# Optimization experiments

Measured on AMD Instinct MI355X. Metric: run time of the kernel, lower is better.

## Reference

```python
import jax, jax.numpy as jnp
import numpy as np

BATCH = 32
LATENT = 128
NODE_DIM = 8
MAX_NODES = 512
H_NODE = 128   # node_generator hidden
H_EDGE = 64    # edge_generator hidden


def setup_inputs() -> dict:
    key = jax.random.key(0)
    ks = jax.random.split(key, 9)
    s = 0.02
    return {
        "z":   jax.random.normal(ks[0], (BATCH, LATENT), dtype=jnp.float32),
        "W1":  jax.random.normal(ks[1], (LATENT, H_NODE), dtype=jnp.float32) * s,
        "b1":  jnp.zeros((H_NODE,), dtype=jnp.float32),
        "W2":  jax.random.normal(ks[2], (H_NODE, MAX_NODES * NODE_DIM), dtype=jnp.float32) * s,
        "b2":  jnp.zeros((MAX_NODES * NODE_DIM,), dtype=jnp.float32),
        "E1":  jax.random.normal(ks[3], (2 * NODE_DIM, H_EDGE), dtype=jnp.float32) * s,
        "eb1": jnp.zeros((H_EDGE,), dtype=jnp.float32),
        "E2":  jax.random.normal(ks[4], (H_EDGE, 1), dtype=jnp.float32) * s,
        "eb2": jnp.zeros((1,), dtype=jnp.float32),
    }


def reference(z, W1, b1, W2, b2, E1, eb1, E2, eb2):
    B = z.shape[0]
    # node generator: Linear -> ReLU -> Linear, view to [B, N, node_dim]
    h = jax.nn.relu(z @ W1 + b1)
    nodes = (h @ W2 + b2).reshape(B, MAX_NODES, NODE_DIM)

    # all unordered pairs i < j (static indices)
    iu, ju = np.triu_indices(MAX_NODES, k=1)  # [P]
    pair = jnp.concatenate([nodes[:, iu, :], nodes[:, ju, :]], axis=-1)  # [B, P, 2d]

    # edge generator: Linear -> ReLU -> Linear -> Sigmoid
    he = jax.nn.relu(jnp.einsum("bpd,dh->bph", pair, E1) + eb1)
    p = jax.nn.sigmoid(jnp.einsum("bph,ho->bpo", he, E2) + eb2)[..., 0]  # [B, P]

    adj = jnp.zeros((B, MAX_NODES, MAX_NODES), dtype=p.dtype)
    adj = adj.at[:, iu, ju].set(p).at[:, ju, iu].set(p)
    return nodes, adj
```

## Files before the change

kernel.cpp:

```cpp
#include <hip/hip_runtime.h>

#define BATCH 32
#define LATENT 128
#define NODE_DIM 8
#define MAX_NODES 512
#define H_NODE 128
#define H_EDGE 64

typedef _Float16 h2 __attribute__((ext_vector_type(2)));

static __device__ __forceinline__ h2 u32_to_h2(unsigned int x) {
    union { unsigned int u; h2 h; } c; c.u = x; return c.h;
}
static __device__ __forceinline__ unsigned int h2_to_u32(h2 x) {
    union { unsigned int u; h2 h; } c; c.h = x; return c.u;
}

#if __has_builtin(__builtin_amdgcn_fdot2)
#define FDOT2(a, b, c) __builtin_amdgcn_fdot2((a), (b), (c), false)
#else
#define FDOT2(a, b, c) ((c) + (float)(a).x * (float)(b).x + (float)(a).y * (float)(b).y)
#endif

#define UPKH_DWORDS (BATCH * 32 * MAX_NODES)

__global__ __launch_bounds__(256) void gen_nodes_uv(
    const float* __restrict__ z,  const float* __restrict__ W1,
    const float* __restrict__ b1, const float* __restrict__ W2,
    const float* __restrict__ b2, const float* __restrict__ E1,
    const float* __restrict__ eb1,
    float* __restrict__ nodes_out, unsigned int* __restrict__ UPKH,
    unsigned int* __restrict__ VH)
{
    const int b      = blockIdx.x;
    const int mslice = blockIdx.y;
    const int tid    = threadIdx.x;
    const int i0     = mslice * 32;

    __shared__ float sz[LATENT];
    __shared__ float sh[H_NODE];
    __shared__ float sE1[2 * NODE_DIM][H_EDGE];
    __shared__ float sEb1[H_EDGE];
    __shared__ float sN[32][NODE_DIM];

    if (tid < LATENT) sz[tid] = z[b * LATENT + tid];
    for (int idx = tid; idx < 2 * NODE_DIM * H_EDGE; idx += 256)
        (&sE1[0][0])[idx] = E1[idx];
    if (tid < H_EDGE) sEb1[tid] = eb1[tid];
    __syncthreads();

    if (tid < H_NODE) {
        float acc = b1[tid];
#pragma unroll 8
        for (int k = 0; k < LATENT; ++k)
            acc += sz[k] * W1[k * H_NODE + tid];
        sh[tid] = fmaxf(acc, 0.0f);
    }
    __syncthreads();

    const int m = mslice * 256 + tid;
    float acc = b2[m];
#pragma unroll 8
    for (int k = 0; k < H_NODE; ++k)
        acc += sh[k] * W2[(size_t)k * (MAX_NODES * NODE_DIM) + m];
    nodes_out[(size_t)b * (MAX_NODES * NODE_DIM) + m] = acc;
    sN[tid >> 3][tid & 7] = acc;
    __syncthreads();

    {
        const int il = tid & 31;
        const int cg = tid >> 5;
#pragma unroll
        for (int rep = 0; rep < 4; ++rep) {
            const int c2 = rep * 8 + cg;
            const int c  = 2 * c2;
            float ua = sEb1[c], ub = sEb1[c + 1];
#pragma unroll
            for (int d = 0; d < NODE_DIM; ++d) {
                const float nd = sN[il][d];
                ua += nd * sE1[d][c];
                ub += nd * sE1[d][c + 1];
            }
            h2 uu = { (_Float16)ua, (_Float16)ub };
            UPKH[((size_t)b * 32 + c2) * MAX_NODES + i0 + il] = h2_to_u32(uu);
        }
    }
    {
        const int jl = tid >> 3;
        const int cq = tid & 7;
#pragma unroll
        for (int rep = 0; rep < 4; ++rep) {
            const int c2 = rep * 8 + cq;
            const int c  = 2 * c2;
            float va = 0.f, vb = 0.f;
#pragma unroll
            for (int d = 0; d < NODE_DIM; ++d) {
                const float nd = sN[jl][d];
                va += nd * sE1[NODE_DIM + d][c];
                vb += nd * sE1[NODE_DIM + d][c + 1];
            }
            h2 vv = { (_Float16)va, (_Float16)vb };
            VH[((size_t)(b * MAX_NODES + i0 + jl) << 5) + c2] = h2_to_u32(vv);
        }
    }
}

__global__ __launch_bounds__(256, 6) void edge_gen(
    const unsigned int* __restrict__ UPKH, const unsigned int* __restrict__ VH,
    const float* __restrict__ E2,  const float* __restrict__ eb2,
    float* __restrict__ adj)
{
    const int b = blockIdx.y;
    int t = blockIdx.x, bi = 0;
    while (t >= 16 - 2 * bi) { t -= 16 - 2 * bi; ++bi; }
    const int jt = 2 * bi + t;
    const bool partial = (jt >> 1) == bi;

    const int tid  = threadIdx.x;
    const int lane = tid & 63;
    const int wv   = tid >> 6;
    const int i0 = bi * 64, j0 = jt * 32;
    const int i  = i0 + lane;

    __shared__ float P[32][65];

    unsigned int uA[32];
#pragma unroll
    for (int c2 = 0; c2 < 32; ++c2)
        uA[c2] = UPKH[((size_t)b * 32 + c2) * MAX_NODES + i];

    unsigned int wb[32];
#pragma unroll
    for (int c2 = 0; c2 < 32; ++c2) {
        h2 w = { (_Float16)E2[2 * c2], (_Float16)E2[2 * c2 + 1] };
        wb[c2] = __builtin_amdgcn_readfirstlane(h2_to_u32(w));
    }

    const float bias = eb2[0];
    float* adjb = adj + (size_t)b * MAX_NODES * MAX_NODES;
    const h2 zh = { (_Float16)0.f, (_Float16)0.f };

#pragma unroll 2
    for (int jj = 0; jj < 8; ++jj) {
        const int jl = wv * 8 + jj;
        const int j  = j0 + jl;
        const int jfl = __builtin_amdgcn_readfirstlane(j);
        const uint4* vrow = (const uint4*)(VH + ((size_t)(b * MAX_NODES + jfl) << 5));

        float a0 = 0.f, a1 = 0.f;
#pragma unroll
        for (int q = 0; q < 8; ++q) {
            const uint4 vv = vrow[q];
#pragma unroll
            for (int k = 0; k < 4; ++k) {
                const int c2 = 4 * q + k;
                unsigned int vu = (k == 0) ? vv.x : (k == 1) ? vv.y
                                : (k == 2) ? vv.z : vv.w;
                const h2 v = u32_to_h2(vu);
                const h2 w = u32_to_h2(wb[c2]);
                h2 s = u32_to_h2(uA[c2]) + v;
                s = __builtin_elementwise_max(s, zh);
                if (k & 1) a1 = FDOT2(s, w, a1);
                else       a0 = FDOT2(s, w, a0);
            }
        }
        const float x = a0 + a1 + bias;
        const float p = __builtin_amdgcn_rcpf(1.0f + __expf(-x));

        if (!partial) {
            adjb[(size_t)j * MAX_NODES + i] = p;
            P[jl][lane] = p;
        } else {
            if (i < j)       { adjb[(size_t)j * MAX_NODES + i] = p;
                               adjb[(size_t)i * MAX_NODES + j] = p; }
            else if (i == j)   adjb[(size_t)j * MAX_NODES + i] = 0.0f;
        }
    }

    if (!partial) {
        __syncthreads();
        const int r = tid & 63;
        const int q = tid >> 6;
        const size_t rowbase = (size_t)(i0 + r) * MAX_NODES + j0 + q * 8;
        float4 o0, o1;
        o0.x = P[q * 8 + 0][r]; o0.y = P[q * 8 + 1][r];
        o0.z = P[q * 8 + 2][r]; o0.w = P[q * 8 + 3][r];
        o1.x = P[q * 8 + 4][r]; o1.y = P[q * 8 + 5][r];
        o1.z = P[q * 8 + 6][r]; o1.w = P[q * 8 + 7][r];
        *(float4*)&adjb[rowbase]     = o0;
        *(float4*)&adjb[rowbase + 4] = o1;
    }
}

extern "C" void kernel_launch(void* const* d_in, const int* in_sizes, int n_in,
                              void* d_out, int out_size, void* d_ws, size_t ws_size,
                              hipStream_t stream)
{
    const float* z   = (const float*)d_in[0];
    const float* W1  = (const float*)d_in[1];
    const float* b1  = (const float*)d_in[2];
    const float* W2  = (const float*)d_in[3];
    const float* b2  = (const float*)d_in[4];
    const float* E1  = (const float*)d_in[5];
    const float* eb1 = (const float*)d_in[6];
    const float* E2  = (const float*)d_in[7];
    const float* eb2 = (const float*)d_in[8];

    float* nodes_out = (float*)d_out;
    float* adj       = (float*)d_out + BATCH * MAX_NODES * NODE_DIM;

    unsigned int* UPKH = (unsigned int*)d_ws;
    unsigned int* VHp  = UPKH + UPKH_DWORDS;

    dim3 g1(BATCH, 16);
    gen_nodes_uv<<<g1, 256, 0, stream>>>(z, W1, b1, W2, b2, E1, eb1,
                                         nodes_out, UPKH, VHp);

    dim3 g2(72, BATCH);
    edge_gen<<<g2, 256, 0, stream>>>(UPKH, VHp, E2, eb2, adj);
}
```

Baseline: 47.91 us.

## Process three tiles per edge block with U reuse and precomputed E2 halves

The edge kernel grid shrinks from 72 to 24 blocks per batch. Each block now walks three tiles taken from a constant tile table and reloads the U registers only when the row tile changes, so per-block setup is amortized. The fp16 conversion of E2 moves into the node kernel and is written to workspace. The trade-off is fewer blocks (768 total) with less latency hiding, an extra barrier per tile, and dropping the occupancy hint from launch_bounds.

```diff
diff --git a/kernel.cpp b/kernel.cpp
--- a/kernel.cpp
+++ b/kernel.cpp
@@ -23,14 +23,26 @@
 #endif
 
 #define UPKH_DWORDS (BATCH * 32 * MAX_NODES)
+#define VH_DWORDS   (BATCH * MAX_NODES * 32)
+
+__device__ const unsigned char TILE_CODE[72] = {
+    0x00,0x01,0x02,0x03,0x04,0x05,0x06,0x07,0x08,0x09,0x0A,0x0B,0x0C,0x0D,0x0E,0x0F,
+    0x12,0x13,0x14,0x15,0x16,0x17,0x18,0x19,0x1A,0x1B,0x1C,0x1D,0x1E,0x1F,
+    0x24,0x25,0x26,0x27,0x28,0x29,0x2A,0x2B,0x2C,0x2D,0x2E,0x2F,
+    0x36,0x37,0x38,0x39,0x3A,0x3B,0x3C,0x3D,0x3E,0x3F,
+    0x48,0x49,0x4A,0x4B,0x4C,0x4D,0x4E,0x4F,
+    0x5A,0x5B,0x5C,0x5D,0x5E,0x5F,
+    0x6C,0x6D,0x6E,0x6F,
+    0x7E,0x7F
+};
 
 __global__ __launch_bounds__(256) void gen_nodes_uv(
     const float* __restrict__ z,  const float* __restrict__ W1,
     const float* __restrict__ b1, const float* __restrict__ W2,
     const float* __restrict__ b2, const float* __restrict__ E1,
-    const float* __restrict__ eb1,
+    const float* __restrict__ eb1, const float* __restrict__ E2,
     float* __restrict__ nodes_out, unsigned int* __restrict__ UPKH,
-    unsigned int* __restrict__ VH)
+    unsigned int* __restrict__ VH, unsigned int* __restrict__ E2H)
 {
     const int b      = blockIdx.x;
     const int mslice = blockIdx.y;
@@ -47,6 +59,11 @@
     for (int idx = tid; idx < 2 * NODE_DIM * H_EDGE; idx += 256)
         (&sE1[0][0])[idx] = E1[idx];
     if (tid < H_EDGE) sEb1[tid] = eb1[tid];
+
+    if (b == 0 && mslice == 0 && tid < 32) {
+        h2 w = { (_Float16)E2[2 * tid], (_Float16)E2[2 * tid + 1] };
+        E2H[tid] = h2_to_u32(w);
+    }
     __syncthreads();
 
     if (tid < H_NODE) {
@@ -105,90 +122,96 @@
     }
 }
 
-__global__ __launch_bounds__(256, 6) void edge_gen(
+__global__ __launch_bounds__(256) void edge_gen(
     const unsigned int* __restrict__ UPKH, const unsigned int* __restrict__ VH,
-    const float* __restrict__ E2,  const float* __restrict__ eb2,
+    const unsigned int* __restrict__ E2H, const float* __restrict__ eb2,
     float* __restrict__ adj)
 {
-    const int b = blockIdx.y;
-    int t = blockIdx.x, bi = 0;
-    while (t >= 16 - 2 * bi) { t -= 16 - 2 * bi; ++bi; }
-    const int jt = 2 * bi + t;
-    const bool partial = (jt >> 1) == bi;
-
+    const int b   = blockIdx.y;
+    const int blk = blockIdx.x;
     const int tid  = threadIdx.x;
     const int lane = tid & 63;
     const int wv   = tid >> 6;
-    const int i0 = bi * 64, j0 = jt * 32;
-    const int i  = i0 + lane;
 
     __shared__ float P[32][65];
 
-    unsigned int uA[32];
-#pragma unroll
-    for (int c2 = 0; c2 < 32; ++c2)
-        uA[c2] = UPKH[((size_t)b * 32 + c2) * MAX_NODES + i];
-
     unsigned int wb[32];
 #pragma unroll
-    for (int c2 = 0; c2 < 32; ++c2) {
-        h2 w = { (_Float16)E2[2 * c2], (_Float16)E2[2 * c2 + 1] };
-        wb[c2] = __builtin_amdgcn_readfirstlane(h2_to_u32(w));
-    }
+    for (int c2 = 0; c2 < 32; ++c2) wb[c2] = E2H[c2];
 
     const float bias = eb2[0];
     float* adjb = adj + (size_t)b * MAX_NODES * MAX_NODES;
     const h2 zh = { (_Float16)0.f, (_Float16)0.f };
 
+    unsigned int uA[32];
+    int cur_bi = -1;
+
+#pragma unroll 1
+    for (int it = 0; it < 3; ++it) {
+        const int code = TILE_CODE[3 * blk + it];
+        const int bi = code >> 4, jt = code & 15;
+        const bool partial = (jt >> 1) == bi;
+        const int i0 = bi * 64, j0 = jt * 32;
+        const int i  = i0 + lane;
+
+        if (bi != cur_bi) {
+            cur_bi = bi;
+#pragma unroll
+            for (int c2 = 0; c2 < 32; ++c2)
+                uA[c2] = UPKH[((size_t)b * 32 + c2) * MAX_NODES + i];
+        }
+
 #pragma unroll 2
-    for (int jj = 0; jj < 8; ++jj) {
-        const int jl = wv * 8 + jj;
-        const int j  = j0 + jl;
-        const int jfl = __builtin_amdgcn_readfirstlane(j);
-        const uint4* vrow = (const uint4*)(VH + ((size_t)(b * MAX_NODES + jfl) << 5));
-
-        float a0 = 0.f, a1 = 0.f;
-#pragma unroll
-        for (int q = 0; q < 8; ++q) {
-            const uint4 vv = vrow[q];
-#pragma unroll
-            for (int k = 0; k < 4; ++k) {
-                const int c2 = 4 * q + k;
-                unsigned int vu = (k == 0) ? vv.x : (k == 1) ? vv.y
-                                : (k == 2) ? vv.z : vv.w;
-                const h2 v = u32_to_h2(vu);
-                const h2 w = u32_to_h2(wb[c2]);
-                h2 s = u32_to_h2(uA[c2]) + v;
-                s = __builtin_elementwise_max(s, zh);
-                if (k & 1) a1 = FDOT2(s, w, a1);
-                else       a0 = FDOT2(s, w, a0);
-            }
-        }
-        const float x = a0 + a1 + bias;
-        const float p = __builtin_amdgcn_rcpf(1.0f + __expf(-x));
+        for (int jj = 0; jj < 8; ++jj) {
+            const int jl = wv * 8 + jj;
+            const int j  = j0 + jl;
+            const int jfl = __builtin_amdgcn_readfirstlane(j);
+            const uint4* vrow = (const uint4*)(VH + ((size_t)(b * MAX_NODES + jfl) << 5));
+
+            float a0 = 0.f, a1 = 0.f;
+#pragma unroll
+            for (int q = 0; q < 8; ++q) {
+                const uint4 vv = vrow[q];
+#pragma unroll
+                for (int k = 0; k < 4; ++k) {
+                    const int c2 = 4 * q + k;
+                    unsigned int vu = (k == 0) ? vv.x : (k == 1) ? vv.y
+                                    : (k == 2) ? vv.z : vv.w;
+                    const h2 v = u32_to_h2(vu);
+                    const h2 w = u32_to_h2(wb[c2]);
+                    h2 s = u32_to_h2(uA[c2]) + v;
+                    s = __builtin_elementwise_max(s, zh);
+                    if (k & 1) a1 = FDOT2(s, w, a1);
+                    else       a0 = FDOT2(s, w, a0);
+                }
+            }
+            const float x = a0 + a1 + bias;
+            const float p = __builtin_amdgcn_rcpf(1.0f + __expf(-x));
+
+            if (!partial) {
+                adjb[(size_t)j * MAX_NODES + i] = p;
+                P[jl][lane] = p;
+            } else {
+                if (i < j)       { adjb[(size_t)j * MAX_NODES + i] = p;
+                                   adjb[(size_t)i * MAX_NODES + j] = p; }
+                else if (i == j)   adjb[(size_t)j * MAX_NODES + i] = 0.0f;
+            }
+        }
 
         if (!partial) {
-            adjb[(size_t)j * MAX_NODES + i] = p;
-            P[jl][lane] = p;
-        } else {
-            if (i < j)       { adjb[(size_t)j * MAX_NODES + i] = p;
-                               adjb[(size_t)i * MAX_NODES + j] = p; }
-            else if (i == j)   adjb[(size_t)j * MAX_NODES + i] = 0.0f;
-        }
-    }
-
-    if (!partial) {
-        __syncthreads();
-        const int r = tid & 63;
-        const int q = tid >> 6;
-        const size_t rowbase = (size_t)(i0 + r) * MAX_NODES + j0 + q * 8;
-        float4 o0, o1;
-        o0.x = P[q * 8 + 0][r]; o0.y = P[q * 8 + 1][r];
-        o0.z = P[q * 8 + 2][r]; o0.w = P[q * 8 + 3][r];
-        o1.x = P[q * 8 + 4][r]; o1.y = P[q * 8 + 5][r];
-        o1.z = P[q * 8 + 6][r]; o1.w = P[q * 8 + 7][r];
-        *(float4*)&adjb[rowbase]     = o0;
-        *(float4*)&adjb[rowbase + 4] = o1;
+            __syncthreads();
+            const int r = tid & 63;
+            const int q = tid >> 6;
+            const size_t rowbase = (size_t)(i0 + r) * MAX_NODES + j0 + q * 8;
+            float4 o0, o1;
+            o0.x = P[q * 8 + 0][r]; o0.y = P[q * 8 + 1][r];
+            o0.z = P[q * 8 + 2][r]; o0.w = P[q * 8 + 3][r];
+            o1.x = P[q * 8 + 4][r]; o1.y = P[q * 8 + 5][r];
+            o1.z = P[q * 8 + 6][r]; o1.w = P[q * 8 + 7][r];
+            *(float4*)&adjb[rowbase]     = o0;
+            *(float4*)&adjb[rowbase + 4] = o1;
+            __syncthreads();
+        }
     }
 }
 
@@ -211,11 +234,12 @@
 
     unsigned int* UPKH = (unsigned int*)d_ws;
     unsigned int* VHp  = UPKH + UPKH_DWORDS;
+    unsigned int* E2H  = VHp + VH_DWORDS;
 
     dim3 g1(BATCH, 16);
-    gen_nodes_uv<<<g1, 256, 0, stream>>>(z, W1, b1, W2, b2, E1, eb1,
-                                         nodes_out, UPKH, VHp);
-
-    dim3 g2(72, BATCH);
-    edge_gen<<<g2, 256, 0, stream>>>(UPKH, VHp, E2, eb2, adj);
-}
+    gen_nodes_uv<<<g1, 256, 0, stream>>>(z, W1, b1, W2, b2, E1, eb1, E2,
+                                         nodes_out, UPKH, VHp, E2H);
+
+    dim3 g2(24, BATCH);
+    edge_gen<<<g2, 256, 0, stream>>>(UPKH, VHp, E2H, eb2, adj);
+}
```

Result: slower. 53.17 us (+11.0%).
